# Kernel tuning notes

Hardware: AMD Instinct MI355X
Metric: run time of the kernel (lower is better)

## Reference

```python
import jax, jax.numpy as jnp
import numpy as np

N = 50000
E = 800000
NFEAT, NHID, NCLASS = 128, 64, 16


def _spmm(row, col, w, x):
    # out[i] = sum_{e: row[e]==i} w[e] * x[col[e]]  -- sparse adj @ x
    return jax.ops.segment_sum(x[col] * w[:, None], row, num_segments=N)


def _gcn_layer(x, row, col, w, W, b):
    return _spmm(row, col, w, x @ W) + b


def setup_inputs() -> dict:
    key = jax.random.key(0)
    ks = jax.random.split(key, 16)
    glorot = lambda k, fi, fo: jax.random.uniform(k, (fi, fo), jnp.float32, -1.0, 1.0) / jnp.sqrt(fi)
    inp = {
        "x": jax.random.normal(ks[0], (N, NFEAT), jnp.float32),
        "edge_row": jax.random.randint(ks[1], (E,), 0, N, jnp.int32),
        "edge_col": jax.random.randint(ks[2], (E,), 0, N, jnp.int32),
        "edge_weight": jax.random.uniform(ks[3], (E,), jnp.float32),
        "W1": glorot(ks[4], NFEAT, NHID), "b1": jnp.zeros((NHID,), jnp.float32),
        "W2": glorot(ks[5], NHID, NHID), "b2": jnp.zeros((NHID,), jnp.float32),
        "W3": glorot(ks[6], NHID, NHID), "b3": jnp.zeros((NHID,), jnp.float32),
        "W4": glorot(ks[7], NHID, NHID), "b4": jnp.zeros((NHID,), jnp.float32),
        "W5": glorot(ks[8], NHID, NCLASS), "b5": jnp.zeros((NCLASS,), jnp.float32),
    }
    return inp


def reference(x, edge_row, edge_col, edge_weight, W1, b1, W2, b2, W3, b3, W4, b4, W5, b5):
    # Inference mode: dropout is identity.
    e1 = _gcn_layer(x, edge_row, edge_col, edge_weight, W1, b1)
    h = jax.nn.relu(e1)
    e2 = _gcn_layer(h, edge_row, edge_col, edge_weight, W2, b2)
    h = jax.nn.relu(e2)
    e3 = _gcn_layer(h, edge_row, edge_col, edge_weight, W3, b3)
    h = jax.nn.relu(e3)
    e4 = _gcn_layer(h, edge_row, edge_col, edge_weight, W4, b4)
    h = jax.nn.relu(e4)
    e5 = _gcn_layer(h, edge_row, edge_col, edge_weight, W5, b5)
    return (jax.nn.log_softmax(e5, axis=1), e1, e2, e3, e4, e5)
```

## Files before the change

### kernel.cpp

```cpp
#include <hip/hip_runtime.h>
#include <math.h>

#define NN 50000
#define NE 800000
#define NFEAT 128
#define NHID 64
#define NCLASS 16
#define NB_SCAN ((NN + 255) / 256)
#define GB ((NN + 63) / 64)
#define SGRP 4
#define ROWS_PER_SGRP ((NN + SGRP - 1) / SGRP)
#define SCHUNKS 392

__device__ inline unsigned short f2bf(float f) {
    unsigned u = __builtin_bit_cast(unsigned, f);
    u += 0x7fffu + ((u >> 16) & 1u);
    return (unsigned short)(u >> 16);
}
__device__ inline float bf2f(unsigned short h) {
    return __builtin_bit_cast(float, (unsigned)h << 16);
}
__device__ inline float pk_w(unsigned v) { return bf2f((unsigned short)(v >> 16)); }
__device__ inline int pk_c(unsigned v) { return (int)(v & 0xffffu); }


__global__ __launch_bounds__(256) void hist_pack_kernel(const int* __restrict__ erow,
                                                        const int* __restrict__ ecol,
                                                        const float* __restrict__ ew,
                                                        int* __restrict__ deg,
                                                        uint2* __restrict__ rr8, int E) {
    int e = blockIdx.x * 256 + threadIdx.x;
    if (e < E) {
        int r = erow[e];
        int k = atomicAdd(&deg[r], 1);
        uint2 v;
        v.x = ((unsigned)r << 16) | (unsigned)k;
        v.y = ((unsigned)f2bf(ew[e]) << 16) | (unsigned)ecol[e];
        rr8[e] = v;
    }
}

__global__ __launch_bounds__(256) void scan_sum_kernel(const int* __restrict__ deg,
                                                       int* __restrict__ blocksum, int n) {
    __shared__ int s[256];
    const int t = threadIdx.x;
    int i = blockIdx.x * 256 + t;
    s[t] = (i < n) ? deg[i] : 0;
    __syncthreads();
#pragma unroll
    for (int off = 128; off > 0; off >>= 1) {
        if (t < off) s[t] += s[t + off];
        __syncthreads();
    }
    if (t == 0) blocksum[blockIdx.x] = s[0];
}

__global__ __launch_bounds__(256) void scan_final_kernel(const int* __restrict__ deg,
                                                         const int* __restrict__ blocksum,
                                                         int* __restrict__ row_ptr, int n) {
    __shared__ int bs[256];
    __shared__ int s[256];
    const int t = threadIdx.x;
    bs[t] = (t < NB_SCAN) ? blocksum[t] : 0;
    __syncthreads();
    for (int off = 1; off < 256; off <<= 1) {
        int u = (t >= off) ? bs[t - off] : 0;
        __syncthreads();
        bs[t] += u;
        __syncthreads();
    }
    const int blockpre = (blockIdx.x == 0) ? 0 : bs[blockIdx.x - 1];

    int i = blockIdx.x * 256 + t;
    int d = (i < n) ? deg[i] : 0;
    s[t] = d;
    __syncthreads();
    for (int off = 1; off < 256; off <<= 1) {
        int u = (t >= off) ? s[t - off] : 0;
        __syncthreads();
        s[t] += u;
        __syncthreads();
    }
    int excl = blockpre + s[t] - d;
    if (i < n) {
        row_ptr[i] = excl;
        if (i == n - 1) row_ptr[n] = excl + d;
    }
}

__global__ __launch_bounds__(256) void scatter_rank8_kernel(const uint2* __restrict__ rr8,
                                                            const int* __restrict__ row_ptr,
                                                            unsigned* __restrict__ pk, int E) {
    const int g = blockIdx.x & (SGRP - 1);
    const int chunk = blockIdx.x / SGRP;
    const int CH = (E + SCHUNKS - 1) / SCHUNKS;
    const int lo = chunk * CH;
    const int hi = (lo + CH < E) ? lo + CH : E;
    const int rlo = g * ROWS_PER_SGRP;
    const int rhi = (rlo + ROWS_PER_SGRP < NN) ? rlo + ROWS_PER_SGRP : NN;
    for (int e = lo + threadIdx.x; e < hi; e += 256) {
        uint2 v = rr8[e];
        int r = (int)(v.x >> 16);
        if (r >= rlo && r < rhi) {
            pk[row_ptr[r] + (int)(v.x & 0xffffu)] = v.y;
        }
    }
}

template <int K, bool RELU_IN>
__global__ __launch_bounds__(256) void gemm64_kernel(const float* __restrict__ in,
                                                     const float* __restrict__ Wg,
                                                     unsigned short* __restrict__ outb, int M) {
    constexpr int KC = 64;
    __shared__ float xs[KC][68];
    __shared__ float Ws[KC][64];
    const int t = threadIdx.x;
    const int tx = t % 16;
    const int ty = t / 16;
    const int r0 = blockIdx.x * 64;

    float acc[4][4];
#pragma unroll
    for (int i = 0; i < 4; i++)
#pragma unroll
        for (int j = 0; j < 4; j++) acc[i][j] = 0.f;

    for (int k0 = 0; k0 < K; k0 += KC) {
        for (int i = t * 4; i < KC * 64; i += 1024) {
            *(float4*)&Ws[i / 64][i % 64] = *(const float4*)&Wg[(size_t)k0 * 64 + i];
        }
        {
            const int r = t / 4;
            const int q = t % 4;
            const int gr = r0 + r;
#pragma unroll
            for (int i = 0; i < 4; i++) {
                int k = q * 16 + i * 4;
                float4 v;
                if (gr < M)
                    v = *(const float4*)&in[(size_t)gr * K + k0 + k];
                else
                    v = make_float4(0.f, 0.f, 0.f, 0.f);
                if (RELU_IN) {
                    v.x = fmaxf(v.x, 0.f);
                    v.y = fmaxf(v.y, 0.f);
                    v.z = fmaxf(v.z, 0.f);
                    v.w = fmaxf(v.w, 0.f);
                }
                xs[k + 0][r] = v.x;
                xs[k + 1][r] = v.y;
                xs[k + 2][r] = v.z;
                xs[k + 3][r] = v.w;
            }
        }
        __syncthreads();
#pragma unroll 8
        for (int k = 0; k < KC; k++) {
            float4 xv = *(const float4*)&xs[k][ty * 4];
            float4 wv = *(const float4*)&Ws[k][tx * 4];
            acc[0][0] += xv.x * wv.x; acc[0][1] += xv.x * wv.y;
            acc[0][2] += xv.x * wv.z; acc[0][3] += xv.x * wv.w;
            acc[1][0] += xv.y * wv.x; acc[1][1] += xv.y * wv.y;
            acc[1][2] += xv.y * wv.z; acc[1][3] += xv.y * wv.w;
            acc[2][0] += xv.z * wv.x; acc[2][1] += xv.z * wv.y;
            acc[2][2] += xv.z * wv.z; acc[2][3] += xv.z * wv.w;
            acc[3][0] += xv.w * wv.x; acc[3][1] += xv.w * wv.y;
            acc[3][2] += xv.w * wv.z; acc[3][3] += xv.w * wv.w;
        }
        __syncthreads();
    }
#pragma unroll
    for (int i = 0; i < 4; i++) {
        int r = r0 + ty * 4 + i;
        if (r < M) {
            ushort4 u;
            u.x = f2bf(acc[i][0]);
            u.y = f2bf(acc[i][1]);
            u.z = f2bf(acc[i][2]);
            u.w = f2bf(acc[i][3]);
            *(ushort4*)&outb[(size_t)r * 64 + tx * 4] = u;
        }
    }
}

template <int NOUT>
__global__ __launch_bounds__(256) void spmm64_fused_kernel(
    const unsigned short* __restrict__ gb,
    const int* __restrict__ row_ptr,
    const unsigned* __restrict__ pk,
    const float* __restrict__ bias,
    const float* __restrict__ Wn,
    float* __restrict__ e_out,
    unsigned short* __restrict__ nxt,
    int M) {
    __shared__ float Wlt[NOUT][65];
    __shared__ float xs[8][64];
    const int t = threadIdx.x;

    for (int idx = t; idx < 64 * NOUT; idx += 256) {
        int k = idx / NOUT, j = idx % NOUT;
        Wlt[j][k] = Wn[idx];
    }

    const int rb = t >> 5;
    const int f2 = (t & 31) * 2;
    const int r = blockIdx.x * 8 + rb;

    int e = row_ptr[r];
    const int end = row_ptr[r + 1];
    float a0 = 0.f, a1 = 0.f;
    for (; e + 7 < end; e += 8) {
        unsigned q0 = pk[e + 0], q1 = pk[e + 1], q2 = pk[e + 2], q3 = pk[e + 3];
        unsigned q4 = pk[e + 4], q5 = pk[e + 5], q6 = pk[e + 6], q7 = pk[e + 7];
        unsigned g0 = *(const unsigned*)&gb[(size_t)pk_c(q0) * 64 + f2];
        unsigned g1 = *(const unsigned*)&gb[(size_t)pk_c(q1) * 64 + f2];
        unsigned g2 = *(const unsigned*)&gb[(size_t)pk_c(q2) * 64 + f2];
        unsigned g3 = *(const unsigned*)&gb[(size_t)pk_c(q3) * 64 + f2];
        unsigned g4 = *(const unsigned*)&gb[(size_t)pk_c(q4) * 64 + f2];
        unsigned g5 = *(const unsigned*)&gb[(size_t)pk_c(q5) * 64 + f2];
        unsigned g6 = *(const unsigned*)&gb[(size_t)pk_c(q6) * 64 + f2];
        unsigned g7 = *(const unsigned*)&gb[(size_t)pk_c(q7) * 64 + f2];
        a0 += pk_w(q0) * bf2f((unsigned short)(g0 & 0xffffu));
        a1 += pk_w(q0) * bf2f((unsigned short)(g0 >> 16));
        a0 += pk_w(q1) * bf2f((unsigned short)(g1 & 0xffffu));
        a1 += pk_w(q1) * bf2f((unsigned short)(g1 >> 16));
        a0 += pk_w(q2) * bf2f((unsigned short)(g2 & 0xffffu));
        a1 += pk_w(q2) * bf2f((unsigned short)(g2 >> 16));
        a0 += pk_w(q3) * bf2f((unsigned short)(g3 & 0xffffu));
        a1 += pk_w(q3) * bf2f((unsigned short)(g3 >> 16));
        a0 += pk_w(q4) * bf2f((unsigned short)(g4 & 0xffffu));
        a1 += pk_w(q4) * bf2f((unsigned short)(g4 >> 16));
        a0 += pk_w(q5) * bf2f((unsigned short)(g5 & 0xffffu));
        a1 += pk_w(q5) * bf2f((unsigned short)(g5 >> 16));
        a0 += pk_w(q6) * bf2f((unsigned short)(g6 & 0xffffu));
        a1 += pk_w(q6) * bf2f((unsigned short)(g6 >> 16));
        a0 += pk_w(q7) * bf2f((unsigned short)(g7 & 0xffffu));
        a1 += pk_w(q7) * bf2f((unsigned short)(g7 >> 16));
    }
    for (; e < end; e++) {
        unsigned q = pk[e];
        unsigned g = *(const unsigned*)&gb[(size_t)pk_c(q) * 64 + f2];
        a0 += pk_w(q) * bf2f((unsigned short)(g & 0xffffu));
        a1 += pk_w(q) * bf2f((unsigned short)(g >> 16));
    }
    float2 v;
    v.x = a0 + bias[f2];
    v.y = a1 + bias[f2 + 1];
    *(float2*)&e_out[(size_t)r * 64 + f2] = v;
    xs[rb][f2] = fmaxf(v.x, 0.f);
    xs[rb][f2 + 1] = fmaxf(v.y, 0.f);
    __syncthreads();

    if (NOUT == 64) {
        const int rblk = t >> 6;
        const int j = t & 63;
        float acc0 = 0.f, acc1 = 0.f;
#pragma unroll 16
        for (int k = 0; k < 64; k++) {
            float w = Wlt[j][k];
            acc0 += xs[rblk][k] * w;
            acc1 += xs[rblk + 4][k] * w;
        }
        nxt[(size_t)(blockIdx.x * 8 + rblk) * 64 + j] = f2bf(acc0);
        nxt[(size_t)(blockIdx.x * 8 + rblk + 4) * 64 + j] = f2bf(acc1);
    } else {
        if (t < 8 * NOUT) {
            const int rr = t / NOUT;
            const int j = t % NOUT;
            float acc = 0.f;
#pragma unroll 16
            for (int k = 0; k < 64; k++) acc += xs[rr][k] * Wlt[j][k];
            nxt[(size_t)(blockIdx.x * 8 + rr) * NOUT + j] = f2bf(acc);
        }
    }
}

__global__ __launch_bounds__(256) void spmm16_lsm_kernel(const unsigned short* __restrict__ tmpc,
                                                         const int* __restrict__ row_ptr,
                                                         const unsigned* __restrict__ pk,
                                                         const float* __restrict__ bias,
                                                         float* __restrict__ e5,
                                                         float* __restrict__ out0, int M) {
    const int t = threadIdx.x;
    const int wv = __builtin_amdgcn_readfirstlane(t >> 6);
    const int lane = t & 63;
    const int f = lane & 15;
    const int s = lane >> 4;
    const int r = blockIdx.x * 4 + wv;
    if (r >= M) return;

    int e = row_ptr[r];
    const int end = row_ptr[r + 1];
    float acc = 0.f;
    for (; e + 8 <= end; e += 8) {
        unsigned qa = pk[e + s];
        unsigned qb = pk[e + 4 + s];
        acc += pk_w(qa) * bf2f(tmpc[(size_t)pk_c(qa) * 16 + f]);
        acc += pk_w(qb) * bf2f(tmpc[(size_t)pk_c(qb) * 16 + f]);
    }
    if (e + 4 <= end) {
        unsigned q = pk[e + s];
        acc += pk_w(q) * bf2f(tmpc[(size_t)pk_c(q) * 16 + f]);
        e += 4;
    }
    if (s < end - e) {
        unsigned q = pk[e + s];
        acc += pk_w(q) * bf2f(tmpc[(size_t)pk_c(q) * 16 + f]);
    }
    acc += __shfl_xor(acc, 16);
    acc += __shfl_xor(acc, 32);
    float v = acc + bias[f];

    float m = v;
#pragma unroll
    for (int off = 1; off < 16; off <<= 1) m = fmaxf(m, __shfl_xor(m, off, 16));
    float sum = expf(v - m);
#pragma unroll
    for (int off = 1; off < 16; off <<= 1) sum += __shfl_xor(sum, off, 16);
    float ls = logf(sum);
    if (lane < 16) {
        e5[(size_t)r * 16 + f] = v;
        out0[(size_t)r * 16 + f] = v - m - ls;
    }
}


extern "C" void kernel_launch(void* const* d_in, const int* in_sizes, int n_in,
                              void* d_out, int out_size, void* d_ws, size_t ws_size,
                              hipStream_t stream) {
    const float* x = (const float*)d_in[0];
    const int* erow = (const int*)d_in[1];
    const int* ecol = (const int*)d_in[2];
    const float* ew = (const float*)d_in[3];
    const float* W1 = (const float*)d_in[4];
    const float* b1 = (const float*)d_in[5];
    const float* W2 = (const float*)d_in[6];
    const float* b2 = (const float*)d_in[7];
    const float* W3 = (const float*)d_in[8];
    const float* b3 = (const float*)d_in[9];
    const float* W4 = (const float*)d_in[10];
    const float* b4 = (const float*)d_in[11];
    const float* W5 = (const float*)d_in[12];
    const float* b5 = (const float*)d_in[13];

    float* out0 = (float*)d_out;
    float* e1 = out0 + (size_t)NN * NCLASS;
    float* e2 = e1 + (size_t)NN * NHID;
    float* e3 = e2 + (size_t)NN * NHID;
    float* e4 = e3 + (size_t)NN * NHID;
    float* e5 = e4 + (size_t)NN * NHID;

    char* ws = (char*)d_ws;
    unsigned short* tmpA = (unsigned short*)ws; ws += (size_t)NN * NHID * 2;
    unsigned short* tmpB = (unsigned short*)ws; ws += (size_t)NN * NHID * 2;
    unsigned short* tmpc = (unsigned short*)ws; ws += ((size_t)NN * NCLASS * 2 + 255) / 256 * 256;
    int* deg = (int*)ws;      ws += ((size_t)NN * 4 + 255) / 256 * 256;
    int* row_ptr = (int*)ws;  ws += ((size_t)(NN + 1) * 4 + 255) / 256 * 256;
    int* blocksum = (int*)ws; ws += ((size_t)NB_SCAN * 4 + 255) / 256 * 256;
    uint2* rr8 = (uint2*)ws;  ws += (size_t)NE * 8;
    unsigned* pk = (unsigned*)ws; ws += (size_t)NE * 4;

    hipMemsetAsync(deg, 0, (size_t)NN * 4, stream);
    hist_pack_kernel<<<(NE + 255) / 256, 256, 0, stream>>>(erow, ecol, ew, deg, rr8, NE);
    scan_sum_kernel<<<NB_SCAN, 256, 0, stream>>>(deg, blocksum, NN);
    scan_final_kernel<<<NB_SCAN, 256, 0, stream>>>(deg, blocksum, row_ptr, NN);
    scatter_rank8_kernel<<<SGRP * SCHUNKS, 256, 0, stream>>>(rr8, row_ptr, pk, NE);

    gemm64_kernel<NFEAT, false><<<GB, 256, 0, stream>>>(x, W1, tmpA, NN);

    const int FG = NN / 8;
    spmm64_fused_kernel<64><<<FG, 256, 0, stream>>>(tmpA, row_ptr, pk, b1, W2, e1, tmpB, NN);
    spmm64_fused_kernel<64><<<FG, 256, 0, stream>>>(tmpB, row_ptr, pk, b2, W3, e2, tmpA, NN);
    spmm64_fused_kernel<64><<<FG, 256, 0, stream>>>(tmpA, row_ptr, pk, b3, W4, e3, tmpB, NN);
    spmm64_fused_kernel<16><<<FG, 256, 0, stream>>>(tmpB, row_ptr, pk, b4, W5, e4, tmpc, NN);

    spmm16_lsm_kernel<<<(NN + 3) / 4, 256, 0, stream>>>(tmpc, row_ptr, pk, b5, e5, out0, NN);
}
```

Before: 348.2 us.

## Stage block edges in LDS, widen gathers to uint2, drop weight LDS staging

```diff
diff --git a/kernel.cpp b/kernel.cpp
--- a/kernel.cpp
+++ b/kernel.cpp
@@ -11,6 +11,7 @@
 #define SGRP 4
 #define ROWS_PER_SGRP ((NN + SGRP - 1) / SGRP)
 #define SCHUNKS 392
+#define EMAX 1024
 
 __device__ inline unsigned short f2bf(float f) {
     unsigned u = __builtin_bit_cast(unsigned, f);
@@ -184,7 +185,7 @@
 }
 
 template <int NOUT>
-__global__ __launch_bounds__(256) void spmm64_fused_kernel(
+__global__ __launch_bounds__(256, 8) void spmm64_fused_kernel(
     const unsigned short* __restrict__ gb,
     const int* __restrict__ row_ptr,
     const unsigned* __restrict__ pk,
@@ -193,62 +194,108 @@
     float* __restrict__ e_out,
     unsigned short* __restrict__ nxt,
     int M) {
-    __shared__ float Wlt[NOUT][65];
     __shared__ float xs[8][64];
+    __shared__ unsigned epk[EMAX];
     const int t = threadIdx.x;
-
-    for (int idx = t; idx < 64 * NOUT; idx += 256) {
-        int k = idx / NOUT, j = idx % NOUT;
-        Wlt[j][k] = Wn[idx];
-    }
-
+    const int lane = t & 63;
     const int rb = t >> 5;
-    const int f2 = (t & 31) * 2;
-    const int r = blockIdx.x * 8 + rb;
-
-    int e = row_ptr[r];
-    const int end = row_ptr[r + 1];
-    float a0 = 0.f, a1 = 0.f;
-    for (; e + 7 < end; e += 8) {
-        unsigned q0 = pk[e + 0], q1 = pk[e + 1], q2 = pk[e + 2], q3 = pk[e + 3];
-        unsigned q4 = pk[e + 4], q5 = pk[e + 5], q6 = pk[e + 6], q7 = pk[e + 7];
-        unsigned g0 = *(const unsigned*)&gb[(size_t)pk_c(q0) * 64 + f2];
-        unsigned g1 = *(const unsigned*)&gb[(size_t)pk_c(q1) * 64 + f2];
-        unsigned g2 = *(const unsigned*)&gb[(size_t)pk_c(q2) * 64 + f2];
-        unsigned g3 = *(const unsigned*)&gb[(size_t)pk_c(q3) * 64 + f2];
-        unsigned g4 = *(const unsigned*)&gb[(size_t)pk_c(q4) * 64 + f2];
-        unsigned g5 = *(const unsigned*)&gb[(size_t)pk_c(q5) * 64 + f2];
-        unsigned g6 = *(const unsigned*)&gb[(size_t)pk_c(q6) * 64 + f2];
-        unsigned g7 = *(const unsigned*)&gb[(size_t)pk_c(q7) * 64 + f2];
-        a0 += pk_w(q0) * bf2f((unsigned short)(g0 & 0xffffu));
-        a1 += pk_w(q0) * bf2f((unsigned short)(g0 >> 16));
-        a0 += pk_w(q1) * bf2f((unsigned short)(g1 & 0xffffu));
-        a1 += pk_w(q1) * bf2f((unsigned short)(g1 >> 16));
-        a0 += pk_w(q2) * bf2f((unsigned short)(g2 & 0xffffu));
-        a1 += pk_w(q2) * bf2f((unsigned short)(g2 >> 16));
-        a0 += pk_w(q3) * bf2f((unsigned short)(g3 & 0xffffu));
-        a1 += pk_w(q3) * bf2f((unsigned short)(g3 >> 16));
-        a0 += pk_w(q4) * bf2f((unsigned short)(g4 & 0xffffu));
-        a1 += pk_w(q4) * bf2f((unsigned short)(g4 >> 16));
-        a0 += pk_w(q5) * bf2f((unsigned short)(g5 & 0xffffu));
-        a1 += pk_w(q5) * bf2f((unsigned short)(g5 >> 16));
-        a0 += pk_w(q6) * bf2f((unsigned short)(g6 & 0xffffu));
-        a1 += pk_w(q6) * bf2f((unsigned short)(g6 >> 16));
-        a0 += pk_w(q7) * bf2f((unsigned short)(g7 & 0xffffu));
-        a1 += pk_w(q7) * bf2f((unsigned short)(g7 >> 16));
-    }
-    for (; e < end; e++) {
-        unsigned q = pk[e];
-        unsigned g = *(const unsigned*)&gb[(size_t)pk_c(q) * 64 + f2];
-        a0 += pk_w(q) * bf2f((unsigned short)(g & 0xffffu));
-        a1 += pk_w(q) * bf2f((unsigned short)(g >> 16));
-    }
-    float2 v;
-    v.x = a0 + bias[f2];
-    v.y = a1 + bias[f2 + 1];
-    *(float2*)&e_out[(size_t)r * 64 + f2] = v;
-    xs[rb][f2] = fmaxf(v.x, 0.f);
-    xs[rb][f2 + 1] = fmaxf(v.y, 0.f);
+    const int slot = (lane >> 4) & 1;
+    const int fl = (lane & 15) * 4;
+
+    const int blk0 = blockIdx.x * 8;
+    const int base = row_ptr[blk0];
+    const int cnt = row_ptr[blk0 + 8] - base;
+    const bool fits = (cnt <= EMAX);
+    if (fits) {
+        for (int i = t; i < cnt; i += 256) epk[i] = pk[base + i];
+    }
+    __syncthreads();
+
+    const int r = blk0 + rb;
+    float a0 = 0.f, a1 = 0.f, a2 = 0.f, a3 = 0.f;
+
+#define FMA_EDGE(q, g)                                              \
+    {                                                               \
+        float w_ = pk_w(q);                                         \
+        a0 += w_ * bf2f((unsigned short)((g).x & 0xffffu));         \
+        a1 += w_ * bf2f((unsigned short)((g).x >> 16));             \
+        a2 += w_ * bf2f((unsigned short)((g).y & 0xffffu));         \
+        a3 += w_ * bf2f((unsigned short)((g).y >> 16));             \
+    }
+#define GLD(q) (*(const uint2*)&gb[(size_t)pk_c(q) * 64 + fl])
+
+    if (fits) {
+        int le = row_ptr[r] - base;
+        const int lend = row_ptr[r + 1] - base;
+        for (; le + 16 <= lend; le += 16) {
+            unsigned q0 = epk[le + 0 + slot], q1 = epk[le + 2 + slot];
+            unsigned q2 = epk[le + 4 + slot], q3 = epk[le + 6 + slot];
+            unsigned q4 = epk[le + 8 + slot], q5 = epk[le + 10 + slot];
+            unsigned q6 = epk[le + 12 + slot], q7 = epk[le + 14 + slot];
+            uint2 g0 = GLD(q0), g1 = GLD(q1), g2 = GLD(q2), g3 = GLD(q3);
+            uint2 g4 = GLD(q4), g5 = GLD(q5), g6 = GLD(q6), g7 = GLD(q7);
+            FMA_EDGE(q0, g0); FMA_EDGE(q1, g1); FMA_EDGE(q2, g2); FMA_EDGE(q3, g3);
+            FMA_EDGE(q4, g4); FMA_EDGE(q5, g5); FMA_EDGE(q6, g6); FMA_EDGE(q7, g7);
+        }
+        if (le + 8 <= lend) {
+            unsigned q0 = epk[le + 0 + slot], q1 = epk[le + 2 + slot];
+            unsigned q2 = epk[le + 4 + slot], q3 = epk[le + 6 + slot];
+            uint2 g0 = GLD(q0), g1 = GLD(q1), g2 = GLD(q2), g3 = GLD(q3);
+            FMA_EDGE(q0, g0); FMA_EDGE(q1, g1); FMA_EDGE(q2, g2); FMA_EDGE(q3, g3);
+            le += 8;
+        }
+        if (le + 4 <= lend) {
+            unsigned q0 = epk[le + 0 + slot], q1 = epk[le + 2 + slot];
+            uint2 g0 = GLD(q0), g1 = GLD(q1);
+            FMA_EDGE(q0, g0); FMA_EDGE(q1, g1);
+            le += 4;
+        }
+        if (le + 2 <= lend) {
+            unsigned q = epk[le + slot];
+            uint2 g = GLD(q);
+            FMA_EDGE(q, g);
+            le += 2;
+        }
+        if (le < lend && slot == 0) {
+            unsigned q = epk[le];
+            uint2 g = GLD(q);
+            FMA_EDGE(q, g);
+        }
+    } else {
+        int e = row_ptr[r];
+        const int end = row_ptr[r + 1];
+        for (; e + 2 <= end; e += 2) {
+            unsigned q = pk[e + slot];
+            uint2 g = GLD(q);
+            FMA_EDGE(q, g);
+        }
+        if (e < end && slot == 0) {
+            unsigned q = pk[e];
+            uint2 g = GLD(q);
+            FMA_EDGE(q, g);
+        }
+    }
+#undef FMA_EDGE
+#undef GLD
+
+    a0 += __shfl_xor(a0, 16);
+    a1 += __shfl_xor(a1, 16);
+    a2 += __shfl_xor(a2, 16);
+    a3 += __shfl_xor(a3, 16);
+
+    if (slot == 0) {
+        float4 b4 = *(const float4*)&bias[fl];
+        float4 v;
+        v.x = a0 + b4.x;
+        v.y = a1 + b4.y;
+        v.z = a2 + b4.z;
+        v.w = a3 + b4.w;
+        *(float4*)&e_out[(size_t)r * 64 + fl] = v;
+        xs[rb][fl + 0] = fmaxf(v.x, 0.f);
+        xs[rb][fl + 1] = fmaxf(v.y, 0.f);
+        xs[rb][fl + 2] = fmaxf(v.z, 0.f);
+        xs[rb][fl + 3] = fmaxf(v.w, 0.f);
+    }
     __syncthreads();
 
     if (NOUT == 64) {
@@ -257,20 +304,20 @@
         float acc0 = 0.f, acc1 = 0.f;
 #pragma unroll 16
         for (int k = 0; k < 64; k++) {
-            float w = Wlt[j][k];
+            float w = Wn[k * 64 + j];
             acc0 += xs[rblk][k] * w;
             acc1 += xs[rblk + 4][k] * w;
         }
-        nxt[(size_t)(blockIdx.x * 8 + rblk) * 64 + j] = f2bf(acc0);
-        nxt[(size_t)(blockIdx.x * 8 + rblk + 4) * 64 + j] = f2bf(acc1);
+        nxt[(size_t)(blk0 + rblk) * 64 + j] = f2bf(acc0);
+        nxt[(size_t)(blk0 + rblk + 4) * 64 + j] = f2bf(acc1);
     } else {
         if (t < 8 * NOUT) {
             const int rr = t / NOUT;
             const int j = t % NOUT;
             float acc = 0.f;
 #pragma unroll 16
-            for (int k = 0; k < 64; k++) acc += xs[rr][k] * Wlt[j][k];
-            nxt[(size_t)(blockIdx.x * 8 + rr) * NOUT + j] = f2bf(acc);
+            for (int k = 0; k < 64; k++) acc += xs[rr][k] * Wn[k * NOUT + j];
+            nxt[(size_t)(blk0 + rr) * NOUT + j] = f2bf(acc);
         }
     }
 }
```

New measurement: 306.3 us (median of 2 runs). 1.14x faster.
